# Kernel tuning notes

Measured on AMD Instinct MI355X. Metric: run time of the kernel, lower is better.

The kernel has to match this reference:

```python
import jax, jax.numpy as jnp
import numpy as np


def setup_inputs() -> dict:
    key = jax.random.key(0)
    k1, k2 = jax.random.split(key)
    b, f, c, h, w = 2, 8, 64, 256, 256
    nbr = jax.random.normal(k1, (b, f, c, h, w), dtype=jnp.float32)
    ref = jax.random.normal(k2, (b, f, c, h, w), dtype=jnp.float32)
    return {"nbr": nbr, "ref": ref}


def reference(nbr, ref):
    # Original: for each query pixel i, sum_j sum_c ref[c,i]*nbr[c,j]
    # computed via chunked QK^T followed by a ones-vector matmul.
    # Identity: weight[..., i] = dot(ref[:, i], sum_j nbr[:, j])
    # -> collapse the O(HW^2) score matrix to a single O(HW*C) contraction.
    k_sum = nbr.sum(axis=(-2, -1))                      # [b, f, c]
    weight = jnp.einsum('bfcxy,bfc->bfxy', ref, k_sum)  # [b, f, h, w]
    weight = jax.nn.sigmoid(weight)
    return weight[:, :, None]                           # [b, f, 1, h, w]
```

## Files before the change

### kernel.cpp

```cpp
#include <hip/hip_runtime.h>
#include <math.h>

#define BF    16
#define CH    64
#define HW    65536

typedef float vfloat4 __attribute__((ext_vector_type(4)));

__global__ __launch_bounds__(256) void ksum_kernel(
    const float* __restrict__ nbr, float* __restrict__ ksum) {
    const int ch  = blockIdx.x;
    const int tid = threadIdx.x;

    const vfloat4* base = (const vfloat4*)(nbr + (size_t)ch * HW);
    float sum = 0.f;
#pragma unroll 8
    for (int k = 0; k < HW / (256 * 4); ++k) {
        vfloat4 v = __builtin_nontemporal_load(&base[tid + k * 256]);
        sum += (v.x + v.y) + (v.z + v.w);
    }
#pragma unroll
    for (int off = 32; off > 0; off >>= 1)
        sum += __shfl_down(sum, off, 64);

    __shared__ float red[4];
    const int lane = tid & 63, wv = tid >> 6;
    if (lane == 0) red[wv] = sum;
    __syncthreads();
    if (tid == 0)
        ksum[ch] = (red[0] + red[1]) + (red[2] + red[3]);
}

__global__ __launch_bounds__(256) void weight_kernel(
    const float* __restrict__ ref, const float* __restrict__ ksum,
    float* __restrict__ out) {
    const int blocksPerBF = HW / (256 * 4);
    const int bf      = blockIdx.x / blocksPerBF;
    const int pix_blk = blockIdx.x % blocksPerBF;
    const int tid     = threadIdx.x;

    __shared__ float ks[CH];
    if (tid < CH)
        ks[tid] = ksum[(size_t)bf * CH + tid];
    __syncthreads();

    const size_t xy0 = (size_t)pix_blk * 1024 + (size_t)tid * 4;
    const float* refbase = ref + (size_t)bf * CH * HW + xy0;

    vfloat4 acc0 = {0.f, 0.f, 0.f, 0.f};
    vfloat4 acc1 = {0.f, 0.f, 0.f, 0.f};
#pragma unroll 8
    for (int c = 0; c < CH; c += 2) {
        vfloat4 r0 = __builtin_nontemporal_load(
            (const vfloat4*)(refbase + (size_t)c * HW));
        vfloat4 r1 = __builtin_nontemporal_load(
            (const vfloat4*)(refbase + (size_t)(c + 1) * HW));
        const float k0 = ks[c], k1 = ks[c + 1];
        acc0.x = fmaf(r0.x, k0, acc0.x);
        acc0.y = fmaf(r0.y, k0, acc0.y);
        acc0.z = fmaf(r0.z, k0, acc0.z);
        acc0.w = fmaf(r0.w, k0, acc0.w);
        acc1.x = fmaf(r1.x, k1, acc1.x);
        acc1.y = fmaf(r1.y, k1, acc1.y);
        acc1.z = fmaf(r1.z, k1, acc1.z);
        acc1.w = fmaf(r1.w, k1, acc1.w);
    }

    vfloat4 o;
    o.x = 1.f / (1.f + __expf(-(acc0.x + acc1.x)));
    o.y = 1.f / (1.f + __expf(-(acc0.y + acc1.y)));
    o.z = 1.f / (1.f + __expf(-(acc0.z + acc1.z)));
    o.w = 1.f / (1.f + __expf(-(acc0.w + acc1.w)));

    __builtin_nontemporal_store(o, (vfloat4*)(out + (size_t)bf * HW + xy0));
}

extern "C" void kernel_launch(void* const* d_in, const int* in_sizes, int n_in,
                              void* d_out, int out_size, void* d_ws, size_t ws_size,
                              hipStream_t stream) {
    const float* nbr = (const float*)d_in[0];
    const float* ref = (const float*)d_in[1];
    float* out       = (float*)d_out;
    float* ksum      = (float*)d_ws;

    ksum_kernel<<<BF * CH, 256, 0, stream>>>(nbr, ksum);
    weight_kernel<<<BF * (HW / 1024), 256, 0, stream>>>(ref, ksum, out);
}
```

Before: 474.3 us.

## Fuse ksum and weight kernels into one cooperative kernel with grid sync

```diff
diff --git a/kernel.cpp b/kernel.cpp
--- a/kernel.cpp
+++ b/kernel.cpp
@@ -1,4 +1,5 @@
 #include <hip/hip_runtime.h>
+#include <hip/hip_cooperative_groups.h>
 #include <math.h>
 
 #define BF    16
@@ -7,11 +8,84 @@
 
 typedef float vfloat4 __attribute__((ext_vector_type(4)));
 
+__global__ __launch_bounds__(256) void fused_kernel(
+    const float* __restrict__ nbr, const float* __restrict__ ref,
+    float* __restrict__ out, float* __restrict__ ksum) {
+    const int tid = threadIdx.x;
+
+    {
+        const int ch = blockIdx.x;
+        const vfloat4* base = (const vfloat4*)(nbr + (size_t)ch * HW);
+        float sum = 0.f;
+#pragma unroll 16
+        for (int k = 0; k < HW / (256 * 4); ++k) {
+            vfloat4 v = __builtin_nontemporal_load(&base[tid + k * 256]);
+            sum += (v.x + v.y) + (v.z + v.w);
+        }
+#pragma unroll
+        for (int off = 32; off > 0; off >>= 1)
+            sum += __shfl_down(sum, off, 64);
+
+        __shared__ float red[4];
+        const int lane = tid & 63, wv = tid >> 6;
+        if (lane == 0) red[wv] = sum;
+        __syncthreads();
+        if (tid == 0) {
+            float v = (red[0] + red[1]) + (red[2] + red[3]);
+            __hip_atomic_store(&ksum[ch], v, __ATOMIC_RELEASE,
+                               __HIP_MEMORY_SCOPE_AGENT);
+        }
+    }
+
+    cooperative_groups::this_grid().sync();
+
+    {
+        const int bf      = blockIdx.x >> 6;
+        const int pix_blk = blockIdx.x & 63;
+
+        __shared__ float ks[CH];
+        if (tid < CH)
+            ks[tid] = __hip_atomic_load(&ksum[(size_t)bf * CH + tid],
+                                        __ATOMIC_ACQUIRE,
+                                        __HIP_MEMORY_SCOPE_AGENT);
+        __syncthreads();
+
+        const size_t xy0 = (size_t)pix_blk * 1024 + (size_t)tid * 4;
+        const float* refbase = ref + (size_t)bf * CH * HW + xy0;
+
+        vfloat4 acc0 = {0.f, 0.f, 0.f, 0.f};
+        vfloat4 acc1 = {0.f, 0.f, 0.f, 0.f};
+#pragma unroll 8
+        for (int c = 0; c < CH; c += 2) {
+            vfloat4 r0 = __builtin_nontemporal_load(
+                (const vfloat4*)(refbase + (size_t)c * HW));
+            vfloat4 r1 = __builtin_nontemporal_load(
+                (const vfloat4*)(refbase + (size_t)(c + 1) * HW));
+            const float k0 = ks[c], k1 = ks[c + 1];
+            acc0.x = fmaf(r0.x, k0, acc0.x);
+            acc0.y = fmaf(r0.y, k0, acc0.y);
+            acc0.z = fmaf(r0.z, k0, acc0.z);
+            acc0.w = fmaf(r0.w, k0, acc0.w);
+            acc1.x = fmaf(r1.x, k1, acc1.x);
+            acc1.y = fmaf(r1.y, k1, acc1.y);
+            acc1.z = fmaf(r1.z, k1, acc1.z);
+            acc1.w = fmaf(r1.w, k1, acc1.w);
+        }
+
+        vfloat4 o;
+        o.x = 1.f / (1.f + __expf(-(acc0.x + acc1.x)));
+        o.y = 1.f / (1.f + __expf(-(acc0.y + acc1.y)));
+        o.z = 1.f / (1.f + __expf(-(acc0.z + acc1.z)));
+        o.w = 1.f / (1.f + __expf(-(acc0.w + acc1.w)));
+
+        __builtin_nontemporal_store(o, (vfloat4*)(out + (size_t)bf * HW + xy0));
+    }
+}
+
 __global__ __launch_bounds__(256) void ksum_kernel(
     const float* __restrict__ nbr, float* __restrict__ ksum) {
     const int ch  = blockIdx.x;
     const int tid = threadIdx.x;
-
     const vfloat4* base = (const vfloat4*)(nbr + (size_t)ch * HW);
     float sum = 0.f;
 #pragma unroll 8
@@ -22,7 +96,6 @@
 #pragma unroll
     for (int off = 32; off > 0; off >>= 1)
         sum += __shfl_down(sum, off, 64);
-
     __shared__ float red[4];
     const int lane = tid & 63, wv = tid >> 6;
     if (lane == 0) red[wv] = sum;
@@ -83,6 +156,11 @@
     float* out       = (float*)d_out;
     float* ksum      = (float*)d_ws;
 
-    ksum_kernel<<<BF * CH, 256, 0, stream>>>(nbr, ksum);
-    weight_kernel<<<BF * (HW / 1024), 256, 0, stream>>>(ref, ksum, out);
+    void* args[] = {(void*)&nbr, (void*)&ref, (void*)&out, (void*)&ksum};
+    hipError_t err = hipLaunchCooperativeKernel(
+        (const void*)fused_kernel, dim3(BF * CH), dim3(256), args, 0, stream);
+    if (err != hipSuccess) {
+        ksum_kernel<<<BF * CH, 256, 0, stream>>>(nbr, ksum);
+        weight_kernel<<<BF * (HW / 1024), 256, 0, stream>>>(ref, ksum, out);
+    }
 }
```

Result: slower. 654.3 us (+37.9%).
